# Kernel optimization log

Measured on AMD Instinct MI355X. Metric: run time of the kernel, lower is better.

Reference implementation:

```python
import jax, jax.numpy as jnp
import numpy as np


def _im2col(x, hf, wf, pad, dilation):
    """Dilated im2col, stride 1, CS231n layout.

    x: (N, C, H, W) -> cols: (C, hf*wf, H*W*N) where the last axis is ordered
    (h, w, n), i.e. index = (h*W + w)*N + n, matching the torch im2col_indices
    helper used by Infuse.
    """
    n, c, h, w = x.shape
    xp = jnp.pad(x, ((0, 0), (0, 0), (pad, pad), (pad, pad)))
    # fixed small loop over the hf*wf window offsets (25 for ksize=5)
    patches = jnp.stack(
        [xp[:, :, i * dilation:i * dilation + h, j * dilation:j * dilation + w]
         for i in range(hf) for j in range(wf)], axis=2)  # (N, C, K2, H, W)
    return patches.transpose(1, 2, 3, 4, 0).reshape(c, hf * wf, h * w * n)


def setup_inputs() -> dict:
    key = jax.random.key(0)
    k1, k2, k3 = jax.random.split(key, 3)
    N, D, H, W, K = 2, 64, 128, 128, 5
    V = jax.random.normal(k1, (N, D, H, W), dtype=jnp.float32)
    boundary = jax.random.uniform(k2, (N, 1, H, W), dtype=jnp.float32)
    dist_to_center = jax.random.uniform(k3, (K * K,), dtype=jnp.float32)
    return {"V": V, "boundary": boundary, "ksize": 5, "dilation": 3,
            "dist_to_center": dist_to_center}


def reference(V, boundary, ksize, dilation, dist_to_center):
    n, d, h, w = V.shape
    pad = (ksize // 2) * dilation
    k2 = ksize * ksize

    # im2col_boundary: gather dilated boundary patches and weight each window
    # offset by its distance to the window center (clipped to a valid boundary
    # probability in [0, 1]).
    bcols = _im2col(boundary, ksize, ksize, pad, dilation)[0]  # (K2, H*W*N)
    boundary_max = jnp.clip(bcols * dist_to_center[:, None], 0.0, 1.0)

    # boundary-proximity attention over the local window
    boundary_sim = 1.0 - boundary_max + 1e-5                   # (K2, H*W*N)
    att = boundary_sim / jnp.sum(boundary_sim, axis=0, keepdims=True)
    # zero-out (scale down) attention at pixels that are themselves boundary
    att = att * (1.0 - boundary).transpose(1, 2, 3, 0).reshape(-1)[None, :]

    # gather feature patches and reduce over the window
    vcols = _im2col(V, ksize, ksize, pad, dilation)            # (D, K2, H*W*N)
    out = (vcols * att[None]).sum(axis=1)                      # (D, H*W*N)
    return out.reshape(d, h, w, n).transpose(3, 0, 1, 2)       # (N, D, H, W)
```

## Files before the change

kernel.cpp:

```cpp
#include <hip/hip_runtime.h>

constexpr int N = 2, D = 64, H = 128, W = 128;
constexpr int K = 5, K2 = 25, DIL = 3, PAD = 6;
constexpr int DCHUNK = 16;
constexpr int HW = H * W;
constexpr int VBYTES = N * D * H * W * 4;
constexpr int SKW = 144;

typedef float float4v __attribute__((ext_vector_type(4)));
typedef float float2v __attribute__((ext_vector_type(2)));

__device__ __forceinline__ int sidx(int w) { return w + 4 * (w >> 5); }

__device__ __forceinline__ void pk_fma(float2v& d, float2v s0, float2v s1) {
    asm("v_pk_fma_f32 %0, %1, %2, %0" : "+v"(d) : "v"(s0), "v"(s1));
}

template<int KLO, int KHI>
__device__ __forceinline__ float phase1_part(const float* __restrict__ bp,
                                             const float* __restrict__ dist,
                                             int h, int w, float* sa) {
    constexpr int KN = KHI - KLO;
    float bvr[KN];
    bool  okk[KN];
#pragma unroll
    for (int kk = 0; kk < KN; ++kk) {
        const int k = KLO + kk, i = k / K, j = k % K;
        int bh = h + i * DIL - PAD;
        int bw = w + j * DIL - PAD;
        okk[kk] = (bh >= 0) & (bh < H) & (bw >= 0) & (bw < W);
        int off = bh * W + bw;
        off = min(max(off, 0), HW - 1);
        bvr[kk] = bp[off];
    }
    float partial = 0.f;
#pragma unroll
    for (int kk = 0; kk < KN; ++kk) {
        const int k = KLO + kk;
        float bv = okk[kk] ? bvr[kk] : 0.f;
        float bm = fminf(fmaxf(bv * dist[k], 0.f), 1.f);
        float s = 1.f - bm + 1e-5f;
        partial += s;
        sa[k * SKW + sidx(w)] = okk[kk] ? s : 0.f;
    }
    return partial;
}

__global__ __launch_bounds__(256, 4)
void infuse_kernel(const float* __restrict__ V,
                   const float* __restrict__ boundary,
                   const float* __restrict__ dist,
                   float* __restrict__ out) {
    int obid = blockIdx.x;
    int bid  = (obid & 7) * 128 + (obid >> 3);
    int dblk = bid & 3;
    int h    = (bid >> 2) & (H-1);
    int n    = bid >> 9;

    __shared__ float s_att[K2 * SKW];
    __shared__ float s_psum[2][W];
    __shared__ float s_scale[W];

    int tid = threadIdx.x;

    int g  = tid & 15;
    int c  = tid >> 4;
    int d  = dblk * DCHUNK + c;
    int gw = 8 * g;
    int sg = sidx(gw);

    int cb   = (n * D + d) * (H * W * 4);
    int colb = gw * 4 - 32;
    const char* Vb = (const char*)V;

    float4v pre[2][6];
#pragma unroll
    for (int i = 0; i < 2; ++i) {
        int r  = h + i * DIL - PAD;
        int rb = cb + r * (W * 4) + colb;
#pragma unroll
        for (int e = 0; e < 6; ++e) {
            int o = rb + 16 * e;
            o = min(max(o, 0), VBYTES - 16);
            pre[i][e] = *(const float4v*)(Vb + o);
        }
    }
    __builtin_amdgcn_sched_barrier(0);

    {
        int w = tid & (W - 1);
        int q = tid >> 7;
        const float* bp = boundary + n * HW;
        float bc = bp[h * W + w];
        float partial = q ? phase1_part<13, 25>(bp, dist, h, w, s_att)
                          : phase1_part<0, 13>(bp, dist, h, w, s_att);
        s_psum[q][w] = partial;
        __syncthreads();
        if (tid < W) {
            float total = s_psum[0][tid] + s_psum[1][tid];
            s_scale[tid] = (1.f - bc) / total;
        }
    }
    __syncthreads();

    float2v acc2[4] = {{0,0},{0,0},{0,0},{0,0}};

#pragma unroll
    for (int i = 0; i < K; ++i) {
        float4v v[6];
        if (i < 2) {
#pragma unroll
            for (int e = 0; e < 6; ++e) v[e] = pre[i][e];
        } else {
            int r  = h + i * DIL - PAD;
            int rb = cb + r * (W * 4) + colb;
#pragma unroll
            for (int e = 0; e < 6; ++e) {
                int o = rb + 16 * e;
                o = min(max(o, 0), VBYTES - 16);
                v[e] = *(const float4v*)(Vb + o);
            }
        }
#pragma unroll
        for (int j = 0; j < K; ++j) {
            const float* ap = &s_att[(i * K + j) * SKW + sg];
            float4v aLo = *(const float4v*)ap;
            float4v aHi = *(const float4v*)(ap + 4);
            if ((j & 1) == 0) {
#pragma unroll
                for (int pp = 0; pp < 4; ++pp) {
                    const int idx = 2 * pp + 3 * j + 2;
                    float2v s0 = {v[idx >> 2][idx & 3],
                                  v[(idx + 1) >> 2][(idx + 1) & 3]};
                    float2v a2 = (pp < 2) ? float2v{aLo[2*pp], aLo[2*pp+1]}
                                          : float2v{aHi[2*pp-4], aHi[2*pp-3]};
                    pk_fma(acc2[pp], s0, a2);
                }
            } else {
#pragma unroll
                for (int px = 0; px < 8; ++px) {
                    const int idx = px + 3 * j + 2;
                    float a = (px < 4) ? aLo[px & 3] : aHi[px & 3];
                    acc2[px >> 1][px & 1] =
                        fmaf(v[idx >> 2][idx & 3], a, acc2[px >> 1][px & 1]);
                }
            }
        }
    }

    float4v scLo = *(const float4v*)&s_scale[gw];
    float4v scHi = *(const float4v*)&s_scale[gw + 4];
    float4v o0 = {acc2[0][0] * scLo[0], acc2[0][1] * scLo[1],
                  acc2[1][0] * scLo[2], acc2[1][1] * scLo[3]};
    float4v o1 = {acc2[2][0] * scHi[0], acc2[2][1] * scHi[1],
                  acc2[3][0] * scHi[2], acc2[3][1] * scHi[3]};

    size_t ob = ((size_t)(n * D + d) * H + h) * W + gw;
    *(float4v*)(out + ob)     = o0;
    *(float4v*)(out + ob + 4) = o1;
}

extern "C" void kernel_launch(void* const* d_in, const int* in_sizes, int n_in,
                              void* d_out, int out_size, void* d_ws, size_t ws_size,
                              hipStream_t stream) {
    const float* V        = (const float*)d_in[0];
    const float* boundary = (const float*)d_in[1];
    const float* dist     = (const float*)d_in[4];
    float* out = (float*)d_out;

    int grid = N * H * (D / DCHUNK);
    infuse_kernel<<<grid, 256, 0, stream>>>(V, boundary, dist, out);
}
```

Baseline: 12.37 us.

## Halve block size, compute 16 pixels per thread with double-buffered row loads

Each block now runs 128 threads instead of 256. Each thread accumulates 16 output pixels instead of 8, so every V row load and attention vector load is reused across more outputs. V row loads are double-buffered: the next kernel row is fetched while the current one is consumed, replacing the fixed two-row prefetch. The boundary/attention phase now has one thread per column computing all 25 window offsets, which removes the partial-sum shared array and one barrier. The cost is more registers per thread, a longer serial attention phase per thread, and fewer waves in flight to hide memory latency.

```diff
diff --git a/kernel.cpp b/kernel.cpp
--- a/kernel.cpp
+++ b/kernel.cpp
@@ -46,7 +46,7 @@
     return partial;
 }
 
-__global__ __launch_bounds__(256, 4)
+__global__ __launch_bounds__(128, 4)
 void infuse_kernel(const float* __restrict__ V,
                    const float* __restrict__ boundary,
                    const float* __restrict__ dist,
@@ -54,93 +54,86 @@
     int obid = blockIdx.x;
     int bid  = (obid & 7) * 128 + (obid >> 3);
     int dblk = bid & 3;
-    int h    = (bid >> 2) & (H-1);
+    int h    = (bid >> 2) & (H - 1);
     int n    = bid >> 9;
 
     __shared__ float s_att[K2 * SKW];
-    __shared__ float s_psum[2][W];
-    __shared__ float s_scale[W];
+    __shared__ float s_scale[SKW];
 
     int tid = threadIdx.x;
 
-    int g  = tid & 15;
-    int c  = tid >> 4;
+    int g  = tid & 7;
+    int c  = tid >> 3;
     int d  = dblk * DCHUNK + c;
-    int gw = 8 * g;
+    int gw = 16 * g;
     int sg = sidx(gw);
 
     int cb   = (n * D + d) * (H * W * 4);
     int colb = gw * 4 - 32;
     const char* Vb = (const char*)V;
 
-    float4v pre[2][6];
-#pragma unroll
-    for (int i = 0; i < 2; ++i) {
-        int r  = h + i * DIL - PAD;
+    float4v vbuf[2][8];
+    {
+        int r  = h - PAD;
         int rb = cb + r * (W * 4) + colb;
 #pragma unroll
-        for (int e = 0; e < 6; ++e) {
+        for (int e = 0; e < 8; ++e) {
             int o = rb + 16 * e;
             o = min(max(o, 0), VBYTES - 16);
-            pre[i][e] = *(const float4v*)(Vb + o);
+            vbuf[0][e] = *(const float4v*)(Vb + o);
         }
     }
     __builtin_amdgcn_sched_barrier(0);
 
     {
-        int w = tid & (W - 1);
-        int q = tid >> 7;
+        int w = tid;
         const float* bp = boundary + n * HW;
         float bc = bp[h * W + w];
-        float partial = q ? phase1_part<13, 25>(bp, dist, h, w, s_att)
-                          : phase1_part<0, 13>(bp, dist, h, w, s_att);
-        s_psum[q][w] = partial;
-        __syncthreads();
-        if (tid < W) {
-            float total = s_psum[0][tid] + s_psum[1][tid];
-            s_scale[tid] = (1.f - bc) / total;
-        }
+        float total = phase1_part<0, 13>(bp, dist, h, w, s_att)
+                    + phase1_part<13, 25>(bp, dist, h, w, s_att);
+        s_scale[sidx(w)] = (1.f - bc) / total;
     }
     __syncthreads();
 
-    float2v acc2[4] = {{0,0},{0,0},{0,0},{0,0}};
+    float2v acc2[8] = {{0,0},{0,0},{0,0},{0,0},{0,0},{0,0},{0,0},{0,0}};
 
 #pragma unroll
     for (int i = 0; i < K; ++i) {
-        float4v v[6];
-        if (i < 2) {
-#pragma unroll
-            for (int e = 0; e < 6; ++e) v[e] = pre[i][e];
-        } else {
-            int r  = h + i * DIL - PAD;
+        if (i < K - 1) {
+            int r  = h + (i + 1) * DIL - PAD;
             int rb = cb + r * (W * 4) + colb;
 #pragma unroll
-            for (int e = 0; e < 6; ++e) {
+            for (int e = 0; e < 8; ++e) {
                 int o = rb + 16 * e;
                 o = min(max(o, 0), VBYTES - 16);
-                v[e] = *(const float4v*)(Vb + o);
+                vbuf[(i + 1) & 1][e] = *(const float4v*)(Vb + o);
             }
         }
+        const float4v (&v)[8] = vbuf[i & 1];
+
 #pragma unroll
         for (int j = 0; j < K; ++j) {
             const float* ap = &s_att[(i * K + j) * SKW + sg];
-            float4v aLo = *(const float4v*)ap;
-            float4v aHi = *(const float4v*)(ap + 4);
+            float4v aa[4];
+            aa[0] = *(const float4v*)ap;
+            aa[1] = *(const float4v*)(ap + 4);
+            aa[2] = *(const float4v*)(ap + 8);
+            aa[3] = *(const float4v*)(ap + 12);
             if ((j & 1) == 0) {
 #pragma unroll
-                for (int pp = 0; pp < 4; ++pp) {
+                for (int pp = 0; pp < 8; ++pp) {
                     const int idx = 2 * pp + 3 * j + 2;
                     float2v s0 = {v[idx >> 2][idx & 3],
                                   v[(idx + 1) >> 2][(idx + 1) & 3]};
-                    float2v a2 = (pp < 2) ? float2v{aLo[2*pp], aLo[2*pp+1]}
-                                          : float2v{aHi[2*pp-4], aHi[2*pp-3]};
-                    pk_fma(acc2[pp], s0, a2);
+                    float2v av = {aa[pp >> 1][(2 * pp) & 3],
+                                  aa[pp >> 1][(2 * pp + 1) & 3]};
+                    pk_fma(acc2[pp], s0, av);
                 }
             } else {
 #pragma unroll
-                for (int px = 0; px < 8; ++px) {
+                for (int px = 0; px < 16; ++px) {
                     const int idx = px + 3 * j + 2;
-                    float a = (px < 4) ? aLo[px & 3] : aHi[px & 3];
+                    float a = aa[px >> 2][px & 3];
                     acc2[px >> 1][px & 1] =
                         fmaf(v[idx >> 2][idx & 3], a, acc2[px >> 1][px & 1]);
                 }
@@ -148,16 +141,22 @@
         }
     }
 
-    float4v scLo = *(const float4v*)&s_scale[gw];
-    float4v scHi = *(const float4v*)&s_scale[gw + 4];
-    float4v o0 = {acc2[0][0] * scLo[0], acc2[0][1] * scLo[1],
-                  acc2[1][0] * scLo[2], acc2[1][1] * scLo[3]};
-    float4v o1 = {acc2[2][0] * scHi[0], acc2[2][1] * scHi[1],
-                  acc2[3][0] * scHi[2], acc2[3][1] * scHi[3]};
+    const float* sp = &s_scale[sg];
+    float4v sc[4];
+    sc[0] = *(const float4v*)sp;
+    sc[1] = *(const float4v*)(sp + 4);
+    sc[2] = *(const float4v*)(sp + 8);
+    sc[3] = *(const float4v*)(sp + 12);
 
     size_t ob = ((size_t)(n * D + d) * H + h) * W + gw;
-    *(float4v*)(out + ob)     = o0;
-    *(float4v*)(out + ob + 4) = o1;
+#pragma unroll
+    for (int q = 0; q < 4; ++q) {
+        float4v o = {acc2[2 * q][0]     * sc[q][0],
+                     acc2[2 * q][1]     * sc[q][1],
+                     acc2[2 * q + 1][0] * sc[q][2],
+                     acc2[2 * q + 1][1] * sc[q][3]};
+        *(float4v*)(out + ob + 4 * q) = o;
+    }
 }
 
 extern "C" void kernel_launch(void* const* d_in, const int* in_sizes, int n_in,
@@ -169,5 +168,5 @@
     float* out = (float*)d_out;
 
     int grid = N * H * (D / DCHUNK);
-    infuse_kernel<<<grid, 256, 0, stream>>>(V, boundary, dist, out);
+    infuse_kernel<<<grid, 128, 0, stream>>>(V, boundary, dist, out);
 }
```

Result: slower. 14.45 us (+16.8%).

## Double-buffer V row loads and compute boundary attention in one thread group

Applied to the files above, without the earlier changes.

The V rows now go through a two-slot register ring buffer. Row i+2 is loaded into the slot just used once row i's FMAs finish, so global loads overlap with compute instead of stalling at the start of each row. The boundary attention phase now runs on only the first 128 threads, each doing all 25 taps. This removes the partial-sum shared array and one block barrier, but idles half the block during that phase. Register pressure stays similar, though the compiler's scheduling of the in-loop loads may differ.

```diff
diff --git a/kernel.cpp b/kernel.cpp
--- a/kernel.cpp
+++ b/kernel.cpp
@@ -54,11 +54,10 @@
     int obid = blockIdx.x;
     int bid  = (obid & 7) * 128 + (obid >> 3);
     int dblk = bid & 3;
-    int h    = (bid >> 2) & (H-1);
+    int h    = (bid >> 2) & (H - 1);
     int n    = bid >> 9;
 
     __shared__ float s_att[K2 * SKW];
-    __shared__ float s_psum[2][W];
     __shared__ float s_scale[W];
 
     int tid = threadIdx.x;
@@ -73,7 +72,7 @@
     int colb = gw * 4 - 32;
     const char* Vb = (const char*)V;
 
-    float4v pre[2][6];
+    float4v vbuf[2][6];
 #pragma unroll
     for (int i = 0; i < 2; ++i) {
         int r  = h + i * DIL - PAD;
@@ -82,24 +81,18 @@
         for (int e = 0; e < 6; ++e) {
             int o = rb + 16 * e;
             o = min(max(o, 0), VBYTES - 16);
-            pre[i][e] = *(const float4v*)(Vb + o);
+            vbuf[i][e] = *(const float4v*)(Vb + o);
         }
     }
     __builtin_amdgcn_sched_barrier(0);
 
-    {
-        int w = tid & (W - 1);
-        int q = tid >> 7;
+    if (tid < W) {
+        int w = tid;
         const float* bp = boundary + n * HW;
         float bc = bp[h * W + w];
-        float partial = q ? phase1_part<13, 25>(bp, dist, h, w, s_att)
-                          : phase1_part<0, 13>(bp, dist, h, w, s_att);
-        s_psum[q][w] = partial;
-        __syncthreads();
-        if (tid < W) {
-            float total = s_psum[0][tid] + s_psum[1][tid];
-            s_scale[tid] = (1.f - bc) / total;
-        }
+        float total = phase1_part<0, 13>(bp, dist, h, w, s_att)
+                    + phase1_part<13, 25>(bp, dist, h, w, s_att);
+        s_scale[w] = (1.f - bc) / total;
     }
     __syncthreads();
 
@@ -107,20 +100,8 @@
 
 #pragma unroll
     for (int i = 0; i < K; ++i) {
-        float4v v[6];
-        if (i < 2) {
-#pragma unroll
-            for (int e = 0; e < 6; ++e) v[e] = pre[i][e];
-        } else {
-            int r  = h + i * DIL - PAD;
-            int rb = cb + r * (W * 4) + colb;
-#pragma unroll
-            for (int e = 0; e < 6; ++e) {
-                int o = rb + 16 * e;
-                o = min(max(o, 0), VBYTES - 16);
-                v[e] = *(const float4v*)(Vb + o);
-            }
-        }
+        const float4v (&v)[6] = vbuf[i & 1];
+
 #pragma unroll
         for (int j = 0; j < K; ++j) {
             const float* ap = &s_att[(i * K + j) * SKW + sg];
@@ -144,6 +125,17 @@
                     acc2[px >> 1][px & 1] =
                         fmaf(v[idx >> 2][idx & 3], a, acc2[px >> 1][px & 1]);
                 }
+            }
+        }
+
+        if (i < K - 2) {
+            int r  = h + (i + 2) * DIL - PAD;
+            int rb = cb + r * (W * 4) + colb;
+#pragma unroll
+            for (int e = 0; e < 6; ++e) {
+                int o = rb + 16 * e;
+                o = min(max(o, 0), VBYTES - 16);
+                vbuf[i & 1][e] = *(const float4v*)(Vb + o);
             }
         }
     }
```

After: 12.80 us. +3.5%, slower.

## Make attention computation wave-local and drop block barriers

Applied to the files above, without the earlier changes.

Each wavefront now computes boundary attention only for the 32 pixels it consumes and stores it in a per-wave LDS slice. A wave shuffle replaces the shared partial-sum array, and the normalization scale is folded into the stored weights. This removes the block-level __syncthreads calls and the final scale multiply. The cost is that the per-wave layout and the correctness of the LDS wait rely on wave-local ordering.

```diff
diff --git a/kernel.cpp b/kernel.cpp
--- a/kernel.cpp
+++ b/kernel.cpp
@@ -5,45 +5,14 @@
 constexpr int DCHUNK = 16;
 constexpr int HW = H * W;
 constexpr int VBYTES = N * D * H * W * 4;
-constexpr int SKW = 144;
+constexpr int SK2 = 36;
+constexpr int WATT = 26 * SK2;
 
 typedef float float4v __attribute__((ext_vector_type(4)));
 typedef float float2v __attribute__((ext_vector_type(2)));
 
-__device__ __forceinline__ int sidx(int w) { return w + 4 * (w >> 5); }
-
 __device__ __forceinline__ void pk_fma(float2v& d, float2v s0, float2v s1) {
     asm("v_pk_fma_f32 %0, %1, %2, %0" : "+v"(d) : "v"(s0), "v"(s1));
-}
-
-template<int KLO, int KHI>
-__device__ __forceinline__ float phase1_part(const float* __restrict__ bp,
-                                             const float* __restrict__ dist,
-                                             int h, int w, float* sa) {
-    constexpr int KN = KHI - KLO;
-    float bvr[KN];
-    bool  okk[KN];
-#pragma unroll
-    for (int kk = 0; kk < KN; ++kk) {
-        const int k = KLO + kk, i = k / K, j = k % K;
-        int bh = h + i * DIL - PAD;
-        int bw = w + j * DIL - PAD;
-        okk[kk] = (bh >= 0) & (bh < H) & (bw >= 0) & (bw < W);
-        int off = bh * W + bw;
-        off = min(max(off, 0), HW - 1);
-        bvr[kk] = bp[off];
-    }
-    float partial = 0.f;
-#pragma unroll
-    for (int kk = 0; kk < KN; ++kk) {
-        const int k = KLO + kk;
-        float bv = okk[kk] ? bvr[kk] : 0.f;
-        float bm = fminf(fmaxf(bv * dist[k], 0.f), 1.f);
-        float s = 1.f - bm + 1e-5f;
-        partial += s;
-        sa[k * SKW + sidx(w)] = okk[kk] ? s : 0.f;
-    }
-    return partial;
 }
 
 __global__ __launch_bounds__(256, 4)
@@ -54,23 +23,23 @@
     int obid = blockIdx.x;
     int bid  = (obid & 7) * 128 + (obid >> 3);
     int dblk = bid & 3;
-    int h    = (bid >> 2) & (H-1);
+    int h    = (bid >> 2) & (H - 1);
     int n    = bid >> 9;
 
-    __shared__ float s_att[K2 * SKW];
-    __shared__ float s_psum[2][W];
-    __shared__ float s_scale[W];
+    __shared__ float s_att[4 * WATT];
 
-    int tid = threadIdx.x;
+    int tid  = threadIdx.x;
+    int wv   = tid >> 6;
+    int lane = tid & 63;
+    float* watt = &s_att[wv * WATT];
 
-    int g  = tid & 15;
-    int c  = tid >> 4;
-    int d  = dblk * DCHUNK + c;
-    int gw = 8 * g;
-    int sg = sidx(gw);
+    int g   = lane & 3;
+    int c   = lane >> 2;
+    int d   = dblk * DCHUNK + c;
+    int px0 = 32 * wv + 8 * g;
 
     int cb   = (n * D + d) * (H * W * 4);
-    int colb = gw * 4 - 32;
+    int colb = px0 * 4 - 32;
     const char* Vb = (const char*)V;
 
     float4v pre[2][6];
@@ -88,22 +57,55 @@
     __builtin_amdgcn_sched_barrier(0);
 
     {
-        int w = tid & (W - 1);
-        int q = tid >> 7;
+        int pxl  = lane & 31;
+        int wpx  = 32 * wv + pxl;
+        int half = lane >> 5;
         const float* bp = boundary + n * HW;
-        float bc = bp[h * W + w];
-        float partial = q ? phase1_part<13, 25>(bp, dist, h, w, s_att)
-                          : phase1_part<0, 13>(bp, dist, h, w, s_att);
-        s_psum[q][w] = partial;
-        __syncthreads();
-        if (tid < W) {
-            float total = s_psum[0][tid] + s_psum[1][tid];
-            s_scale[tid] = (1.f - bc) / total;
+        float bc = bp[h * W + wpx];
+
+        float bvr[13];
+        bool  ok[13];
+#pragma unroll
+        for (int kk = 0; kk < 13; ++kk) {
+            const int iA = kk / 5,        jA = kk % 5;
+            const int iB = (kk + 13) / 5, jB = (kk + 13) % 5;
+            int idel = half ? (iB * DIL - PAD) : (iA * DIL - PAD);
+            int jdel = half ? (jB * DIL - PAD) : (jA * DIL - PAD);
+            int bh = h + idel;
+            int bw = wpx + jdel;
+            bool inb = (bh >= 0) & (bh < H) & (bw >= 0) & (bw < W);
+            if (kk == 12) inb = inb & (half == 0);
+            ok[kk] = inb;
+            int off = bh * W + bw;
+            off = min(max(off, 0), HW - 1);
+            bvr[kk] = bp[off];
         }
+        float sv[13];
+        float partial = 0.f;
+#pragma unroll
+        for (int kk = 0; kk < 13; ++kk) {
+            float dA = dist[kk];
+            float dB = (kk < 12) ? dist[kk + 13] : 0.f;
+            float dk = half ? dB : dA;
+            float bv = ok[kk] ? bvr[kk] : 0.f;
+            float bm = fminf(fmaxf(bv * dk, 0.f), 1.f);
+            float s  = 1.f - bm + 1e-5f;
+            partial += (kk == 12) ? (half ? 0.f : s) : s;
+            sv[kk] = s;
+        }
+        float other = __shfl_xor(partial, 32);
+        float total = partial + other;
+        float scale = (1.f - bc) / total;
+        float* sb = watt + half * 13 * SK2 + pxl;
+#pragma unroll
+        for (int kk = 0; kk < 13; ++kk)
+            sb[kk * SK2] = ok[kk] ? sv[kk] * scale : 0.f;
     }
-    __syncthreads();
+    asm volatile("s_waitcnt lgkmcnt(0)" ::: "memory");
+    __builtin_amdgcn_sched_barrier(0);
 
     float2v acc2[4] = {{0,0},{0,0},{0,0},{0,0}};
+    const float* ar = watt + 8 * g;
 
 #pragma unroll
     for (int i = 0; i < K; ++i) {
@@ -123,7 +125,7 @@
         }
 #pragma unroll
         for (int j = 0; j < K; ++j) {
-            const float* ap = &s_att[(i * K + j) * SKW + sg];
+            const float* ap = ar + (i * K + j) * SK2;
             float4v aLo = *(const float4v*)ap;
             float4v aHi = *(const float4v*)(ap + 4);
             if ((j & 1) == 0) {
@@ -148,14 +150,10 @@
         }
     }
 
-    float4v scLo = *(const float4v*)&s_scale[gw];
-    float4v scHi = *(const float4v*)&s_scale[gw + 4];
-    float4v o0 = {acc2[0][0] * scLo[0], acc2[0][1] * scLo[1],
-                  acc2[1][0] * scLo[2], acc2[1][1] * scLo[3]};
-    float4v o1 = {acc2[2][0] * scHi[0], acc2[2][1] * scHi[1],
-                  acc2[3][0] * scHi[2], acc2[3][1] * scHi[3]};
+    float4v o0 = {acc2[0][0], acc2[0][1], acc2[1][0], acc2[1][1]};
+    float4v o1 = {acc2[2][0], acc2[2][1], acc2[3][0], acc2[3][1]};
 
-    size_t ob = ((size_t)(n * D + d) * H + h) * W + gw;
+    size_t ob = ((size_t)(n * D + d) * H + h) * W + px0;
     *(float4v*)(out + ob)     = o0;
     *(float4v*)(out + ob + 4) = o1;
 }
```

After: 12.38 us. About the same (+0.1%).
